# Optimization experiments

Hardware: AMD Instinct MI355X
Metric: run time of the kernel (lower is better)

## Reference

```python
import jax, jax.numpy as jnp
import numpy as np

NP, NT, H, FT, E, EL = 200000, 100000, 64, 64, 2000000, 500000


def _seg_mean(msg, dst, n):
    s = jax.ops.segment_sum(msg, dst, num_segments=n)
    c = jax.ops.segment_sum(jnp.ones(dst.shape, msg.dtype), dst, num_segments=n)
    return s / jnp.maximum(c, 1.0)[:, None]


def _sage(x_src, x_dst, src, dst, wl, bl, wr):
    # PyG SAGEConv (aggr='mean'): lin_l(mean_neighbors) + lin_r(x_dst); lin_r has no bias
    mean = _seg_mean(x_src[src], dst, x_dst.shape[0])
    return mean @ wl + bl + x_dst @ wr


def setup_inputs() -> dict:
    key = jax.random.key(0)
    ks = jax.random.split(key, 24)
    s = 1.0 / np.sqrt(H)
    inp = {
        "x_taxon": jax.random.normal(ks[0], (NT, FT), jnp.float32),
        "taxon_lin_w": jax.random.normal(ks[1], (FT, H), jnp.float32) * (1.0 / np.sqrt(FT)),
        "taxon_lin_b": jax.random.normal(ks[2], (H,), jnp.float32) * 0.01,
        "palmprint_emb": jax.random.normal(ks[3], (NP, H), jnp.float32),
        "taxon_emb": jax.random.normal(ks[4], (NT, H), jnp.float32),
        "n_id_palmprint": jnp.arange(NP, dtype=jnp.int64),
        "n_id_taxon": jnp.arange(NT, dtype=jnp.int64),
        "edge_src": jax.random.randint(ks[5], (E,), 0, NP, jnp.int64),
        "edge_dst": jax.random.randint(ks[6], (E,), 0, NT, jnp.int64),
        "el_src": jax.random.randint(ks[7], (EL,), 0, NP, jnp.int64),
        "el_dst": jax.random.randint(ks[8], (EL,), 0, NT, jnp.int64),
    }
    names = ["c1pt_wl", "c1pt_wr", "c1tp_wl", "c1tp_wr", "c2pt_wl", "c2pt_wr", "c2tp_wl", "c2tp_wr"]
    for i, nm in enumerate(names):
        inp[nm] = jax.random.normal(ks[9 + i], (H, H), jnp.float32) * s
    for i, nm in enumerate(["c1pt_bl", "c1tp_bl", "c2pt_bl", "c2tp_bl"]):
        inp[nm] = jax.random.normal(ks[17 + i], (H,), jnp.float32) * 0.01
    return inp


def reference(x_taxon, taxon_lin_w, taxon_lin_b, palmprint_emb, taxon_emb,
              c1pt_wl, c1pt_wr, c1tp_wl, c1tp_wr, c2pt_wl, c2pt_wr, c2tp_wl, c2tp_wr,
              c1pt_bl, c1tp_bl, c2pt_bl, c2tp_bl,
              n_id_palmprint, n_id_taxon, edge_src, edge_dst, el_src, el_dst):
    # initial features (use_embeddings=True)
    x_p = palmprint_emb[n_id_palmprint]                       # [NP, H]
    x_t = x_taxon @ taxon_lin_w + taxon_lin_b + taxon_emb[n_id_taxon]  # [NT, H]

    # layer 1: p->t and t->p (reverse edges), then ReLU
    t1 = _sage(x_p, x_t, edge_src, edge_dst, c1pt_wl, c1pt_bl, c1pt_wr)
    p1 = _sage(x_t, x_p, edge_dst, edge_src, c1tp_wl, c1tp_bl, c1tp_wr)
    p1, t1 = jax.nn.relu(p1), jax.nn.relu(t1)

    # layer 2
    t2 = _sage(p1, t1, edge_src, edge_dst, c2pt_wl, c2pt_bl, c2pt_wr)
    p2 = _sage(t1, p1, edge_dst, edge_src, c2tp_wl, c2tp_bl, c2tp_wr)

    # classifier: per-supervision-edge dot product
    return jnp.sum(p2[el_src] * t2[el_dst], axis=-1)          # [EL]
```

## Files before the change

### kernel.cpp

```cpp
#include <hip/hip_runtime.h>

#define H 64
#define EPB 4096
#define BMAX 400
#define ST 256
#define SP 512
#define LSHT 18
#define LSHP 17
#define CAPB 5632

typedef _Float16 half2v __attribute__((ext_vector_type(2)));
typedef _Float16 half8v __attribute__((ext_vector_type(8)));
typedef _Float16 f16x8  __attribute__((ext_vector_type(8)));
typedef float    f32x4  __attribute__((ext_vector_type(4)));
typedef int      i32x4  __attribute__((ext_vector_type(4)));

#if defined(__has_builtin)
#if __has_builtin(__builtin_amdgcn_fdot2)
#define HAS_FDOT2 1
#endif
#endif

#define MFMA16(a, b, c) __builtin_amdgcn_mfma_f32_16x16x32_f16(a, b, c, 0, 0, 0)

template <int HALF_IN>
__device__ __forceinline__ void mfma_dual_dev(const void* __restrict__ Av,
                                              const float* __restrict__ W1,
                                              const float* __restrict__ W2,
                                              const float* __restrict__ b2,
                                              _Float16* __restrict__ C1,
                                              _Float16* __restrict__ C2,
                                              int N, int wid, int nwaves) {
    const int lane = threadIdx.x & 63;
    const int m = lane & 15, quad = lane >> 4;
    const int nTiles = (N + 15) >> 4;

    f16x8 w1f[2][4], w2f[2][4];
#pragma unroll
    for (int kh = 0; kh < 2; ++kh)
#pragma unroll
        for (int nt = 0; nt < 4; ++nt) {
            f16x8 a, b;
#pragma unroll
            for (int j = 0; j < 8; ++j) {
                int k = kh * 32 + quad * 8 + j;
                a[j] = (_Float16)W1[k * 64 + nt * 16 + m];
                b[j] = (_Float16)W2[k * 64 + nt * 16 + m];
            }
            w1f[kh][nt] = a;
            w2f[kh][nt] = b;
        }
    float bv[4];
#pragma unroll
    for (int nt = 0; nt < 4; ++nt) bv[nt] = b2[nt * 16 + m];

    for (int t = wid; t < nTiles; t += nwaves) {
        int row = t * 16 + m;
        f16x8 alo = {}, ahi = {};
        if (row < N) {
            if (HALF_IN) {
                const f16x8* A8 = (const f16x8*)Av;
                alo = __builtin_nontemporal_load(A8 + (size_t)row * 8 + quad);
                ahi = __builtin_nontemporal_load(A8 + (size_t)row * 8 + 4 + quad);
            } else {
                const f32x4* p = (const f32x4*)((const float*)Av + (size_t)row * 64);
                f32x4 x0 = __builtin_nontemporal_load(p + quad * 2);
                f32x4 x1 = __builtin_nontemporal_load(p + quad * 2 + 1);
                f32x4 x2 = __builtin_nontemporal_load(p + 8 + quad * 2);
                f32x4 x3 = __builtin_nontemporal_load(p + 8 + quad * 2 + 1);
                alo[0] = (_Float16)x0[0]; alo[1] = (_Float16)x0[1];
                alo[2] = (_Float16)x0[2]; alo[3] = (_Float16)x0[3];
                alo[4] = (_Float16)x1[0]; alo[5] = (_Float16)x1[1];
                alo[6] = (_Float16)x1[2]; alo[7] = (_Float16)x1[3];
                ahi[0] = (_Float16)x2[0]; ahi[1] = (_Float16)x2[1];
                ahi[2] = (_Float16)x2[2]; ahi[3] = (_Float16)x2[3];
                ahi[4] = (_Float16)x3[0]; ahi[5] = (_Float16)x3[1];
                ahi[6] = (_Float16)x3[2]; ahi[7] = (_Float16)x3[3];
            }
        }
#pragma unroll
        for (int nt = 0; nt < 4; ++nt) {
            f32x4 a1 = {0.f, 0.f, 0.f, 0.f}, a2 = {0.f, 0.f, 0.f, 0.f};
            a1 = MFMA16(alo, w1f[0][nt], a1);
            a1 = MFMA16(ahi, w1f[1][nt], a1);
            a2 = MFMA16(alo, w2f[0][nt], a2);
            a2 = MFMA16(ahi, w2f[1][nt], a2);
#pragma unroll
            for (int r = 0; r < 4; ++r) {
                int orow = t * 16 + quad * 4 + r;
                if (orow < N) {
                    C1[(size_t)orow * 64 + nt * 16 + m] = (_Float16)a1[r];
                    C2[(size_t)orow * 64 + nt * 16 + m] = (_Float16)(a2[r] + bv[nt]);
                }
            }
        }
    }
}

__device__ __forceinline__ void mfma_xt_dev(const float* __restrict__ A,
                                            const float* __restrict__ W,
                                            const float* __restrict__ bias,
                                            const float* __restrict__ addend,
                                            _Float16* __restrict__ C,
                                            int N, int wid, int nwaves) {
    const int lane = threadIdx.x & 63;
    const int m = lane & 15, quad = lane >> 4;
    const int nTiles = (N + 15) >> 4;

    f16x8 wf[2][4];
#pragma unroll
    for (int kh = 0; kh < 2; ++kh)
#pragma unroll
        for (int nt = 0; nt < 4; ++nt) {
            f16x8 a;
#pragma unroll
            for (int j = 0; j < 8; ++j) {
                int k = kh * 32 + quad * 8 + j;
                a[j] = (_Float16)W[k * 64 + nt * 16 + m];
            }
            wf[kh][nt] = a;
        }
    float bv[4];
#pragma unroll
    for (int nt = 0; nt < 4; ++nt) bv[nt] = bias[nt * 16 + m];

    for (int t = wid; t < nTiles; t += nwaves) {
        int row = t * 16 + m;
        f16x8 alo = {}, ahi = {};
        if (row < N) {
            const f32x4* p = (const f32x4*)(A + (size_t)row * 64);
            f32x4 x0 = __builtin_nontemporal_load(p + quad * 2);
            f32x4 x1 = __builtin_nontemporal_load(p + quad * 2 + 1);
            f32x4 x2 = __builtin_nontemporal_load(p + 8 + quad * 2);
            f32x4 x3 = __builtin_nontemporal_load(p + 8 + quad * 2 + 1);
            alo[0] = (_Float16)x0[0]; alo[1] = (_Float16)x0[1];
            alo[2] = (_Float16)x0[2]; alo[3] = (_Float16)x0[3];
            alo[4] = (_Float16)x1[0]; alo[5] = (_Float16)x1[1];
            alo[6] = (_Float16)x1[2]; alo[7] = (_Float16)x1[3];
            ahi[0] = (_Float16)x2[0]; ahi[1] = (_Float16)x2[1];
            ahi[2] = (_Float16)x2[2]; ahi[3] = (_Float16)x2[3];
            ahi[4] = (_Float16)x3[0]; ahi[5] = (_Float16)x3[1];
            ahi[6] = (_Float16)x3[2]; ahi[7] = (_Float16)x3[3];
        }
#pragma unroll
        for (int nt = 0; nt < 4; ++nt) {
            f32x4 a1 = {0.f, 0.f, 0.f, 0.f};
            a1 = MFMA16(alo, wf[0][nt], a1);
            a1 = MFMA16(ahi, wf[1][nt], a1);
#pragma unroll
            for (int r = 0; r < 4; ++r) {
                int orow = t * 16 + quad * 4 + r;
                if (orow < N) {
                    float ad = __builtin_nontemporal_load(
                        &addend[(size_t)orow * 64 + nt * 16 + m]);
                    C[(size_t)orow * 64 + nt * 16 + m] = (_Float16)(a1[r] + bv[nt] + ad);
                }
            }
        }
    }
}

__device__ __forceinline__ void block_scan512(int* sc, int tid) {
    for (int off = 1; off < 512; off <<= 1) {
        int i0 = tid, i1 = tid + 256;
        int v0 = (i0 >= off) ? sc[i0 - off] : 0;
        int v1 = (i1 >= off) ? sc[i1 - off] : 0;
        __syncthreads();
        sc[i0] += v0;
        sc[i1] += v1;
        __syncthreads();
    }
}

__global__ void __launch_bounds__(256) k_bin_xt(
    const int* __restrict__ src, const int* __restrict__ dst,
    int* __restrict__ curT, int* __restrict__ curP,
    unsigned* __restrict__ binT, unsigned* __restrict__ binP,
    int BT, int BP, int E, int nbBin,
    const float* __restrict__ A, const float* __restrict__ W,
    const float* __restrict__ bias, const float* __restrict__ addend,
    _Float16* __restrict__ C, int NT_, int xtBlocks) {
    __shared__ int cT[BMAX], cP[BMAX], oT[BMAX], oP[BMAX], cur[BMAX];
    __shared__ int sc[512];
    __shared__ unsigned stage[EPB];
    int tid = threadIdx.x;
    if ((int)blockIdx.x >= nbBin) {
        int xb = blockIdx.x - nbBin;
        mfma_xt_dev(A, W, bias, addend, C, NT_, xb * 4 + (tid >> 6), xtBlocks * 4);
        return;
    }
    const int wave = tid >> 6, lane = tid & 63;
    for (int i = tid; i < BMAX; i += 256) { cT[i] = 0; cP[i] = 0; }
    __syncthreads();
    int e0 = blockIdx.x * EPB;
    int ls[EPB / 256], ld[EPB / 256];
#pragma unroll
    for (int k = 0; k < EPB / 256; ++k) {
        int i = e0 + k * 256 + tid;
        if (i < E) {
            ls[k] = __builtin_nontemporal_load(&src[i]);
            ld[k] = __builtin_nontemporal_load(&dst[i]);
            atomicAdd(&cT[ld[k] >> 8], 1);
            atomicAdd(&cP[ls[k] >> 9], 1);
        }
    }
    __syncthreads();
    for (int b = tid; b < BT; b += 256) { int c = cT[b]; oT[b] = c ? atomicAdd(&curT[b], c) : 0; }
    for (int b = tid; b < BP; b += 256) { int c = cP[b]; oP[b] = c ? atomicAdd(&curP[b], c) : 0; }
    sc[tid]       = (tid < BT) ? cT[tid] : 0;
    sc[tid + 256] = (tid + 256 < BT) ? cT[tid + 256] : 0;
    __syncthreads();
    block_scan512(sc, tid);
    for (int b = tid; b < BT; b += 256) cur[b] = sc[b] - cT[b];
    __syncthreads();
#pragma unroll
    for (int k = 0; k < EPB / 256; ++k) {
        int i = e0 + k * 256 + tid;
        if (i < E) {
            int bt = ld[k] >> 8;
            int pos = atomicAdd(&cur[bt], 1);
            stage[pos] = ((unsigned)(ld[k] & 255) << LSHT) | (unsigned)ls[k];
        }
    }
    __syncthreads();
    for (int b = wave; b < BT; b += 4) {
        int cnt = cT[b], so = sc[b] - cnt, go = oT[b];
        for (int i = lane; i < cnt; i += 64) {
            int pos = go + i;
            if (pos < CAPB) binT[(size_t)b * CAPB + pos] = stage[so + i];
        }
    }
    __syncthreads();
    sc[tid]       = (tid < BP) ? cP[tid] : 0;
    sc[tid + 256] = (tid + 256 < BP) ? cP[tid + 256] : 0;
    __syncthreads();
    block_scan512(sc, tid);
    for (int b = tid; b < BP; b += 256) cur[b] = sc[b] - cP[b];
    __syncthreads();
#pragma unroll
    for (int k = 0; k < EPB / 256; ++k) {
        int i = e0 + k * 256 + tid;
        if (i < E) {
            int bp = ls[k] >> 9;
            int pos = atomicAdd(&cur[bp], 1);
            stage[pos] = ((unsigned)(ls[k] & 511) << LSHP) | (unsigned)ld[k];
        }
    }
    __syncthreads();
    for (int b = wave; b < BP; b += 4) {
        int cnt = cP[b], so = sc[b] - cnt, go = oP[b];
        for (int i = lane; i < cnt; i += 64) {
            int pos = go + i;
            if (pos < CAPB) binP[(size_t)b * CAPB + pos] = stage[so + i];
        }
    }
}

__device__ __forceinline__ void csr_dev(const unsigned* __restrict__ binned,
                                        const int* __restrict__ cur,
                                        int* __restrict__ start_g, int* __restrict__ cnt_g,
                                        int* __restrict__ adj,
                                        int S, int lshift, int N, int b,
                                        int* lcnt, int* lscan, int* lcur, int* adj_lds) {
    int tid = threadIdx.x;
    int base = b * CAPB;
    int n = cur[b]; if (n > CAPB) n = CAPB;
    int rowlo = b * S;
    unsigned nbmask = (1u << lshift) - 1u;

    for (int i = tid; i < S; i += 256) lcnt[i] = 0;
    __syncthreads();
    for (int i = tid; i < n; i += 256)
        atomicAdd(&lcnt[binned[base + i] >> lshift], 1);
    __syncthreads();
    for (int i = tid; i < S; i += 256) lscan[i] = lcnt[i];
    __syncthreads();
    for (int off = 1; off < S; off <<= 1) {
        int i0 = tid, i1 = tid + 256;
        int v0 = (i0 >= off) ? lscan[i0 - off] : 0;
        int v1 = (S > 256 && i1 >= off) ? lscan[i1 - off] : 0;
        __syncthreads();
        if (i0 < S) lscan[i0] += v0;
        if (S > 256 && i1 < S) lscan[i1] += v1;
        __syncthreads();
    }
    for (int r = tid; r < S; r += 256) {
        int ex = lscan[r] - lcnt[r];
        lcur[r] = ex;
        int row = rowlo + r;
        if (row < N) {
            start_g[row] = base + ex;
            cnt_g[row]   = lcnt[r];
        }
    }
    __syncthreads();
    for (int i = tid; i < n; i += 256) {
        unsigned e = binned[base + i];
        int r = e >> lshift;
        int pos = atomicAdd(&lcur[r], 1);
        adj_lds[pos] = (int)(e & nbmask);
    }
    __syncthreads();
    int n4 = n & ~3;
    for (int i = tid * 4; i < n4; i += 1024)
        *(int4*)&adj[base + i] = *(const int4*)&adj_lds[i];
    for (int i = n4 + tid; i < n; i += 256)
        adj[base + i] = adj_lds[i];
}

__global__ void __launch_bounds__(256) k_csr_mfma1(
    const unsigned* __restrict__ binT, const unsigned* __restrict__ binP,
    const int* __restrict__ curT, const int* __restrict__ curP,
    int* __restrict__ start_t, int* __restrict__ cnt_t, int* __restrict__ adj_t,
    int* __restrict__ start_p, int* __restrict__ cnt_p, int* __restrict__ adj_p,
    int BT, int BP, int NT_, int NP_,
    const _Float16* __restrict__ XTh, const float* __restrict__ Wt1, const float* __restrict__ Wt2,
    const float* __restrict__ bt2, _Float16* __restrict__ Aht, _Float16* __restrict__ Bth,
    const float* __restrict__ pemb, const float* __restrict__ Wp1, const float* __restrict__ Wp2,
    const float* __restrict__ bp2, _Float16* __restrict__ Ahp, _Float16* __restrict__ Bph,
    int tB, int pB) {
    __shared__ int lcnt[512], lscan[512], lcur[512];
    __shared__ int adj_lds[CAPB];
    int bi = blockIdx.x;
    if (bi < BT) {
        csr_dev(binT, curT, start_t, cnt_t, adj_t, ST, LSHT, NT_, bi, lcnt, lscan, lcur, adj_lds);
    } else if (bi < BT + BP) {
        csr_dev(binP, curP, start_p, cnt_p, adj_p, SP, LSHP, NP_, bi - BT, lcnt, lscan, lcur, adj_lds);
    } else if (bi < BT + BP + tB) {
        int wb = bi - BT - BP;
        mfma_dual_dev<1>(XTh, Wt1, Wt2, bt2, Aht, Bth, NT_, wb * 4 + (threadIdx.x >> 6), tB * 4);
    } else {
        int wb = bi - BT - BP - tB;
        mfma_dual_dev<0>(pemb, Wp1, Wp2, bp2, Ahp, Bph, NP_, wb * 4 + (threadIdx.x >> 6), pB * 4);
    }
}

__device__ __forceinline__ void stage_w_lds(half8v* ldsW,
                                            const float* __restrict__ W1,
                                            const float* __restrict__ W2, int tid) {
    for (int f = tid; f < 1024; f += 256) {
        int lane = f & 63, nt = (f >> 6) & 3, kh = (f >> 8) & 1, tbl = f >> 9;
        int m = lane & 15, quad = lane >> 4;
        const float* W = tbl ? W2 : W1;
        half8v frag;
#pragma unroll
        for (int j = 0; j < 8; ++j) {
            int k = kh * 32 + quad * 8 + j;
            frag[j] = (_Float16)W[k * 64 + nt * 16 + m];
        }
        ldsW[f] = frag;
    }
}

__device__ __forceinline__ void gather_gemm_dev(
    const int* __restrict__ adj, const int* __restrict__ start, const int* __restrict__ cnt,
    const _Float16* __restrict__ A, const _Float16* __restrict__ B,
    const half8v* __restrict__ ldsW, const float* __restrict__ b2,
    _Float16* __restrict__ C1, _Float16* __restrict__ C2,
    int N, int tile) {
    const int lane = threadIdx.x & 63;
    const int m = lane & 15, quad = lane >> 4;
    const int row = tile * 16 + m;

    half8v accl = {}, acch = {};
    int dg = 0;
    if (row < N) {
        int st = start[row];
        dg     = cnt[row];
        const half8v* A8 = (const half8v*)A;
        int j = 0;
        for (; j + 7 < dg; j += 8) {
            int n[8];
#pragma unroll
            for (int k = 0; k < 8; ++k) n[k] = adj[st + j + k];
            half8v lv[8], hv[8];
#pragma unroll
            for (int k = 0; k < 8; ++k) {
                const half8v* rp = A8 + (size_t)n[k] * 8 + quad;
                lv[k] = rp[0];
                hv[k] = rp[4];
            }
            accl += ((lv[0] + lv[1]) + (lv[2] + lv[3])) + ((lv[4] + lv[5]) + (lv[6] + lv[7]));
            acch += ((hv[0] + hv[1]) + (hv[2] + hv[3])) + ((hv[4] + hv[5]) + (hv[6] + hv[7]));
        }
        if (j + 3 < dg) {
            int n[4];
#pragma unroll
            for (int k = 0; k < 4; ++k) n[k] = adj[st + j + k];
            half8v lv[4], hv[4];
#pragma unroll
            for (int k = 0; k < 4; ++k) {
                const half8v* rp = A8 + (size_t)n[k] * 8 + quad;
                lv[k] = rp[0];
                hv[k] = rp[4];
            }
            accl += (lv[0] + lv[1]) + (lv[2] + lv[3]);
            acch += (hv[0] + hv[1]) + (hv[2] + hv[3]);
            j += 4;
        }
        for (; j < dg; ++j) {
            const half8v* rp = A8 + (size_t)adj[st + j] * 8 + quad;
            accl += rp[0];
            acch += rp[4];
        }
    }

    f16x8 alo = {}, ahi = {};
    if (row < N) {
        float inv = 1.0f / (float)(dg > 1 ? dg : 1);
        half8v bl = __builtin_nontemporal_load(&((const half8v*)B)[(size_t)row * 8 + quad]);
        half8v bh = __builtin_nontemporal_load(&((const half8v*)B)[(size_t)row * 8 + 4 + quad]);
#pragma unroll
        for (int k = 0; k < 8; ++k) {
            float vl = fmaxf((float)accl[k] * inv + (float)bl[k], 0.f);
            float vh = fmaxf((float)acch[k] * inv + (float)bh[k], 0.f);
            alo[k] = (_Float16)vl;
            ahi[k] = (_Float16)vh;
        }
    }

#pragma unroll
    for (int nt = 0; nt < 4; ++nt) {
        f16x8 w1l = (f16x8)ldsW[(0 * 8 + 0 * 4 + nt) * 64 + lane];
        f16x8 w1h = (f16x8)ldsW[(0 * 8 + 1 * 4 + nt) * 64 + lane];
        f16x8 w2l = (f16x8)ldsW[(1 * 8 + 0 * 4 + nt) * 64 + lane];
        f16x8 w2h = (f16x8)ldsW[(1 * 8 + 1 * 4 + nt) * 64 + lane];
        f32x4 a1 = {0.f, 0.f, 0.f, 0.f}, a2 = {0.f, 0.f, 0.f, 0.f};
        a1 = MFMA16(alo, w1l, a1);
        a1 = MFMA16(ahi, w1h, a1);
        a2 = MFMA16(alo, w2l, a2);
        a2 = MFMA16(ahi, w2h, a2);
        float bb = b2[nt * 16 + m];
#pragma unroll
        for (int r = 0; r < 4; ++r) {
            int orow = tile * 16 + quad * 4 + r;
            if (orow < N) {
                C1[(size_t)orow * 64 + nt * 16 + m] = (_Float16)a1[r];
                C2[(size_t)orow * 64 + nt * 16 + m] = (_Float16)(a2[r] + bb);
            }
        }
    }
}

__global__ void __launch_bounds__(256) k_gather_gemm(
    const int* __restrict__ adjT, const int* __restrict__ startT, const int* __restrict__ cntT,
    const _Float16* __restrict__ At, const _Float16* __restrict__ Bt,
    const float* __restrict__ Wt1, const float* __restrict__ Wt2, const float* __restrict__ bt2,
    _Float16* __restrict__ C1t, _Float16* __restrict__ C2t, int NT_,
    const int* __restrict__ adjP, const int* __restrict__ startP, const int* __restrict__ cntP,
    const _Float16* __restrict__ Ap, const _Float16* __restrict__ Bp,
    const float* __restrict__ Wp1, const float* __restrict__ Wp2, const float* __restrict__ bp2,
    _Float16* __restrict__ C1p, _Float16* __restrict__ C2p, int NP_,
    int tTB) {
    __shared__ half8v ldsW[1024];
    const int tid = threadIdx.x, wave = tid >> 6;
    if ((int)blockIdx.x < tTB) {
        stage_w_lds(ldsW, Wt1, Wt2, tid);
        __syncthreads();
        int tile = blockIdx.x * 4 + wave;
        if (tile < ((NT_ + 15) >> 4))
            gather_gemm_dev(adjT, startT, cntT, At, Bt, ldsW, bt2, C1t, C2t, NT_, tile);
    } else {
        stage_w_lds(ldsW, Wp1, Wp2, tid);
        __syncthreads();
        int tile = (blockIdx.x - tTB) * 4 + wave;
        if (tile < ((NP_ + 15) >> 4))
            gather_gemm_dev(adjP, startP, cntP, Ap, Bp, ldsW, bp2, C1p, C2p, NP_, tile);
    }
}

__device__ __forceinline__ void gather_dev(
    const int* __restrict__ adj, const int* __restrict__ start, const int* __restrict__ cnt,
    const _Float16* __restrict__ A, const _Float16* __restrict__ B,
    _Float16* __restrict__ out, int do_relu, int N, int gidx) {
    int row = gidx >> 3;
    int c   = gidx & 7;
    if (row >= N) return;

    int st = start[row];
    int dg = cnt[row];
    const half8v* A8 = (const half8v*)A;
    half8v acc = {};
    int j = 0;
    for (; j + 15 < dg; j += 16) {
        int n[16];
#pragma unroll
        for (int k = 0; k < 16; ++k) n[k] = adj[st + j + k];
        half8v v[16];
#pragma unroll
        for (int k = 0; k < 16; ++k) v[k] = A8[(size_t)n[k] * 8 + c];
        half8v s0 = ((v[0] + v[1]) + (v[2] + v[3])) + ((v[4] + v[5]) + (v[6] + v[7]));
        half8v s1 = ((v[8] + v[9]) + (v[10] + v[11])) + ((v[12] + v[13]) + (v[14] + v[15]));
        acc += s0 + s1;
    }
    if (j + 7 < dg) {
        int n[8];
#pragma unroll
        for (int k = 0; k < 8; ++k) n[k] = adj[st + j + k];
        half8v v[8];
#pragma unroll
        for (int k = 0; k < 8; ++k) v[k] = A8[(size_t)n[k] * 8 + c];
        acc += ((v[0] + v[1]) + (v[2] + v[3])) + ((v[4] + v[5]) + (v[6] + v[7]));
        j += 8;
    }
    if (j + 3 < dg) {
        int n[4];
#pragma unroll
        for (int k = 0; k < 4; ++k) n[k] = adj[st + j + k];
        half8v v[4];
#pragma unroll
        for (int k = 0; k < 4; ++k) v[k] = A8[(size_t)n[k] * 8 + c];
        acc += (v[0] + v[1]) + (v[2] + v[3]);
        j += 4;
    }
    for (; j < dg; ++j)
        acc += A8[(size_t)adj[st + j] * 8 + c];

    float inv = 1.0f / (float)(dg > 1 ? dg : 1);
    half8v b8 = __builtin_nontemporal_load(&((const half8v*)B)[(size_t)row * 8 + c]);
    half8v o;
#pragma unroll
    for (int k = 0; k < 8; ++k) {
        float v = (float)acc[k] * inv + (float)b8[k];
        if (do_relu) v = fmaxf(v, 0.f);
        o[k] = (_Float16)v;
    }
    ((half8v*)out)[(size_t)row * 8 + c] = o;
}

__global__ void __launch_bounds__(256) k_gather2(
    const int* __restrict__ adjT, const int* __restrict__ startT, const int* __restrict__ cntT,
    const _Float16* __restrict__ At, const _Float16* __restrict__ Bt, _Float16* __restrict__ outT, int NT_,
    const int* __restrict__ adjP, const int* __restrict__ startP, const int* __restrict__ cntP,
    const _Float16* __restrict__ Ap, const _Float16* __restrict__ Bp, _Float16* __restrict__ outP, int NP_,
    int do_relu, int wTb) {
    if ((int)blockIdx.x < wTb)
        gather_dev(adjT, startT, cntT, At, Bt, outT, do_relu, NT_, blockIdx.x * 256 + threadIdx.x);
    else
        gather_dev(adjP, startP, cntP, Ap, Bp, outP, do_relu, NP_,
                   (blockIdx.x - wTb) * 256 + threadIdx.x);
}

__global__ void __launch_bounds__(256) dot_h(const _Float16* __restrict__ p2,
                                             const _Float16* __restrict__ t2,
                                             const int* __restrict__ els,
                                             const int* __restrict__ eld,
                                             float* __restrict__ out, int EL) {
    int tid = blockIdx.x * 256 + threadIdx.x;
    int i = tid >> 3, c = tid & 7;
    if (i < EL) {
        int s = __builtin_nontemporal_load(&els[i]);
        int d = __builtin_nontemporal_load(&eld[i]);
        half8v a = ((const half8v*)p2)[(size_t)s * 8 + c];
        half8v b = ((const half8v*)t2)[(size_t)d * 8 + c];
        float v = 0.f;
#ifdef HAS_FDOT2
        const half2v* ap = (const half2v*)&a;
        const half2v* bp = (const half2v*)&b;
#pragma unroll
        for (int k = 0; k < 4; ++k) v = __builtin_amdgcn_fdot2(ap[k], bp[k], v, false);
#else
#pragma unroll
        for (int k = 0; k < 8; ++k) v += (float)a[k] * (float)b[k];
#endif
        v += __shfl_xor(v, 1, 64);
        v += __shfl_xor(v, 2, 64);
        v += __shfl_xor(v, 4, 64);
        if (c == 0) __builtin_nontemporal_store(v, &out[i]);
    }
}

extern "C" void kernel_launch(void* const* d_in, const int* in_sizes, int n_in,
                              void* d_out, int out_size, void* d_ws, size_t ws_size,
                              hipStream_t stream) {
    const float* x_taxon  = (const float*)d_in[0];
    const float* tlw      = (const float*)d_in[1];
    const float* tlb      = (const float*)d_in[2];
    const float* pemb     = (const float*)d_in[3];
    const float* temb     = (const float*)d_in[4];
    const int*   edge_src = (const int*)d_in[7];
    const int*   edge_dst = (const int*)d_in[8];
    const int*   el_src   = (const int*)d_in[9];
    const int*   el_dst   = (const int*)d_in[10];
    const float* c1pt_wl  = (const float*)d_in[11];
    const float* c1pt_wr  = (const float*)d_in[12];
    const float* c1tp_wl  = (const float*)d_in[13];
    const float* c1tp_wr  = (const float*)d_in[14];
    const float* c2pt_wl  = (const float*)d_in[15];
    const float* c2pt_wr  = (const float*)d_in[16];
    const float* c2tp_wl  = (const float*)d_in[17];
    const float* c2tp_wr  = (const float*)d_in[18];
    const float* c1pt_bl  = (const float*)d_in[19];
    const float* c1tp_bl  = (const float*)d_in[20];
    const float* c2pt_bl  = (const float*)d_in[21];
    const float* c2tp_bl  = (const float*)d_in[22];

    const int NP_ = in_sizes[5];
    const int NT_ = in_sizes[6];
    const int E_  = in_sizes[7];
    const int EL_ = in_sizes[9];
    const int BT  = (NT_ + ST - 1) / ST;
    const int BP  = (NP_ + SP - 1) / SP;

    _Float16* hb   = (_Float16*)d_ws;
    _Float16* XTh  = hb;
    _Float16* Aht1 = XTh + (size_t)NT_ * H;
    _Float16* Bth1 = Aht1 + (size_t)NT_ * H;
    _Float16* Bth2 = Bth1 + (size_t)NT_ * H;
    _Float16* Ahp1 = Bth2 + (size_t)NT_ * H;
    _Float16* Bph1 = Ahp1 + (size_t)NP_ * H;
    _Float16* Ahp2 = Bph1 + (size_t)NP_ * H;
    _Float16* Bph2 = Ahp2 + (size_t)NP_ * H;
    _Float16* Aht2 = XTh;
    _Float16* T2h  = Aht1;
    _Float16* P2h  = Ahp1;

    unsigned* binT    = (unsigned*)(Bph2 + (size_t)NP_ * H);
    unsigned* binP    = binT + (size_t)BT * CAPB;
    int*      adj_t   = (int*)(binP + (size_t)BP * CAPB);
    int*      adj_p   = adj_t + (size_t)BT * CAPB;
    int* start_t = adj_p + (size_t)BP * CAPB;
    int* start_p = start_t + NT_;
    int* cnt_t   = start_p + NP_;
    int* cnt_p   = cnt_t + NT_;
    int* curT    = cnt_p + NP_;
    int* curP    = curT + BMAX;

    (void)hipMemsetAsync(curT, 0, 2 * BMAX * sizeof(int), stream);

    const int nbBin = (E_ + EPB - 1) / EPB;
    const int XTB   = 512;
    const int wT = (NT_ * 8 + 255) / 256, wP = (NP_ * 8 + 255) / 256;
    const int tB = 256, pB = 512;

    k_bin_xt<<<nbBin + XTB, 256, 0, stream>>>(
        edge_src, edge_dst, curT, curP, binT, binP, BT, BP, E_, nbBin,
        x_taxon, tlw, tlb, temb, XTh, NT_, XTB);

    k_csr_mfma1<<<BT + BP + tB + pB, 256, 0, stream>>>(
        binT, binP, curT, curP,
        start_t, cnt_t, adj_t, start_p, cnt_p, adj_p, BT, BP, NT_, NP_,
        XTh, c1tp_wl, c1pt_wr, c1pt_bl, Aht1, Bth1,
        pemb, c1pt_wl, c1tp_wr, c1tp_bl, Ahp1, Bph1, tB, pB);

    const int tTB = (((NT_ + 15) >> 4) + 3) >> 2;
    const int pTB = (((NP_ + 15) >> 4) + 3) >> 2;
    k_gather_gemm<<<tTB + pTB, 256, 0, stream>>>(
        adj_t, start_t, cnt_t, Ahp1, Bth1, c2tp_wl, c2pt_wr, c2pt_bl, Aht2, Bth2, NT_,
        adj_p, start_p, cnt_p, Aht1, Bph1, c2pt_wl, c2tp_wr, c2tp_bl, Ahp2, Bph2, NP_,
        tTB);

    k_gather2<<<wT + wP, 256, 0, stream>>>(
        adj_t, start_t, cnt_t, Ahp2, Bth2, T2h, NT_,
        adj_p, start_p, cnt_p, Aht2, Bph2, P2h, NP_, 0, wT);

    dot_h<<<(EL_ * 8 + 255) / 256, 256, 0, stream>>>(P2h, T2h, el_src, el_dst,
                                                     (float*)d_out, EL_);
}
```

Baseline: 476.7 us.

## Aggregate-then-transform both SAGE layers with fused gather-GEMM kernels

The old path projected features through both weight matrices first, then gathered projected rows, and ran a separate gather-only pass for layer 2. Now raw fp16 features are gathered and mean-aggregated, then one fused MFMA applies lin_l and lin_r together, with output staged through LDS for coalesced stores. Palmprint embeddings are cast to fp16 inside the binning kernel, the standalone projection work in the CSR kernel is dropped, and intermediate buffers shrink. This removes a full pass over edges and several intermediate tensors, but the layer-1 gather now waits on CSR completion with no projection overlap.

```diff
diff --git a/kernel.cpp b/kernel.cpp
--- a/kernel.cpp
+++ b/kernel.cpp
@@ -22,80 +22,6 @@
 #endif
 
 #define MFMA16(a, b, c) __builtin_amdgcn_mfma_f32_16x16x32_f16(a, b, c, 0, 0, 0)
-
-template <int HALF_IN>
-__device__ __forceinline__ void mfma_dual_dev(const void* __restrict__ Av,
-                                              const float* __restrict__ W1,
-                                              const float* __restrict__ W2,
-                                              const float* __restrict__ b2,
-                                              _Float16* __restrict__ C1,
-                                              _Float16* __restrict__ C2,
-                                              int N, int wid, int nwaves) {
-    const int lane = threadIdx.x & 63;
-    const int m = lane & 15, quad = lane >> 4;
-    const int nTiles = (N + 15) >> 4;
-
-    f16x8 w1f[2][4], w2f[2][4];
-#pragma unroll
-    for (int kh = 0; kh < 2; ++kh)
-#pragma unroll
-        for (int nt = 0; nt < 4; ++nt) {
-            f16x8 a, b;
-#pragma unroll
-            for (int j = 0; j < 8; ++j) {
-                int k = kh * 32 + quad * 8 + j;
-                a[j] = (_Float16)W1[k * 64 + nt * 16 + m];
-                b[j] = (_Float16)W2[k * 64 + nt * 16 + m];
-            }
-            w1f[kh][nt] = a;
-            w2f[kh][nt] = b;
-        }
-    float bv[4];
-#pragma unroll
-    for (int nt = 0; nt < 4; ++nt) bv[nt] = b2[nt * 16 + m];
-
-    for (int t = wid; t < nTiles; t += nwaves) {
-        int row = t * 16 + m;
-        f16x8 alo = {}, ahi = {};
-        if (row < N) {
-            if (HALF_IN) {
-                const f16x8* A8 = (const f16x8*)Av;
-                alo = __builtin_nontemporal_load(A8 + (size_t)row * 8 + quad);
-                ahi = __builtin_nontemporal_load(A8 + (size_t)row * 8 + 4 + quad);
-            } else {
-                const f32x4* p = (const f32x4*)((const float*)Av + (size_t)row * 64);
-                f32x4 x0 = __builtin_nontemporal_load(p + quad * 2);
-                f32x4 x1 = __builtin_nontemporal_load(p + quad * 2 + 1);
-                f32x4 x2 = __builtin_nontemporal_load(p + 8 + quad * 2);
-                f32x4 x3 = __builtin_nontemporal_load(p + 8 + quad * 2 + 1);
-                alo[0] = (_Float16)x0[0]; alo[1] = (_Float16)x0[1];
-                alo[2] = (_Float16)x0[2]; alo[3] = (_Float16)x0[3];
-                alo[4] = (_Float16)x1[0]; alo[5] = (_Float16)x1[1];
-                alo[6] = (_Float16)x1[2]; alo[7] = (_Float16)x1[3];
-                ahi[0] = (_Float16)x2[0]; ahi[1] = (_Float16)x2[1];
-                ahi[2] = (_Float16)x2[2]; ahi[3] = (_Float16)x2[3];
-                ahi[4] = (_Float16)x3[0]; ahi[5] = (_Float16)x3[1];
-                ahi[6] = (_Float16)x3[2]; ahi[7] = (_Float16)x3[3];
-            }
-        }
-#pragma unroll
-        for (int nt = 0; nt < 4; ++nt) {
-            f32x4 a1 = {0.f, 0.f, 0.f, 0.f}, a2 = {0.f, 0.f, 0.f, 0.f};
-            a1 = MFMA16(alo, w1f[0][nt], a1);
-            a1 = MFMA16(ahi, w1f[1][nt], a1);
-            a2 = MFMA16(alo, w2f[0][nt], a2);
-            a2 = MFMA16(ahi, w2f[1][nt], a2);
-#pragma unroll
-            for (int r = 0; r < 4; ++r) {
-                int orow = t * 16 + quad * 4 + r;
-                if (orow < N) {
-                    C1[(size_t)orow * 64 + nt * 16 + m] = (_Float16)a1[r];
-                    C2[(size_t)orow * 64 + nt * 16 + m] = (_Float16)(a2[r] + bv[nt]);
-                }
-            }
-        }
-    }
-}
 
 __device__ __forceinline__ void mfma_xt_dev(const float* __restrict__ A,
                                             const float* __restrict__ W,
@@ -179,11 +105,30 @@
     int BT, int BP, int E, int nbBin,
     const float* __restrict__ A, const float* __restrict__ W,
     const float* __restrict__ bias, const float* __restrict__ addend,
-    _Float16* __restrict__ C, int NT_, int xtBlocks) {
+    _Float16* __restrict__ C, int NT_, int xtBlocks,
+    const float* __restrict__ pembIn, _Float16* __restrict__ PhOut,
+    int NP_, int castBlocks) {
     __shared__ int cT[BMAX], cP[BMAX], oT[BMAX], oP[BMAX], cur[BMAX];
     __shared__ int sc[512];
     __shared__ unsigned stage[EPB];
     int tid = threadIdx.x;
+    if ((int)blockIdx.x >= nbBin + xtBlocks) {
+        int cb = blockIdx.x - nbBin - xtBlocks;
+        int idx = cb * 256 + tid, stride = castBlocks * 256;
+        int total = NP_ * 8;
+        for (int i = idx; i < total; i += stride) {
+            const f32x4* p = (const f32x4*)(pembIn + (size_t)i * 8);
+            f32x4 x0 = __builtin_nontemporal_load(p);
+            f32x4 x1 = __builtin_nontemporal_load(p + 1);
+            f16x8 o;
+            o[0] = (_Float16)x0[0]; o[1] = (_Float16)x0[1];
+            o[2] = (_Float16)x0[2]; o[3] = (_Float16)x0[3];
+            o[4] = (_Float16)x1[0]; o[5] = (_Float16)x1[1];
+            o[6] = (_Float16)x1[2]; o[7] = (_Float16)x1[3];
+            *(f16x8*)&PhOut[(size_t)i * 8] = o;
+        }
+        return;
+    }
     if ((int)blockIdx.x >= nbBin) {
         int xb = blockIdx.x - nbBin;
         mfma_xt_dev(A, W, bias, addend, C, NT_, xb * 4 + (tid >> 6), xtBlocks * 4);
@@ -308,31 +253,19 @@
         adj[base + i] = adj_lds[i];
 }
 
-__global__ void __launch_bounds__(256) k_csr_mfma1(
+__global__ void __launch_bounds__(256) k_csr(
     const unsigned* __restrict__ binT, const unsigned* __restrict__ binP,
     const int* __restrict__ curT, const int* __restrict__ curP,
     int* __restrict__ start_t, int* __restrict__ cnt_t, int* __restrict__ adj_t,
     int* __restrict__ start_p, int* __restrict__ cnt_p, int* __restrict__ adj_p,
-    int BT, int BP, int NT_, int NP_,
-    const _Float16* __restrict__ XTh, const float* __restrict__ Wt1, const float* __restrict__ Wt2,
-    const float* __restrict__ bt2, _Float16* __restrict__ Aht, _Float16* __restrict__ Bth,
-    const float* __restrict__ pemb, const float* __restrict__ Wp1, const float* __restrict__ Wp2,
-    const float* __restrict__ bp2, _Float16* __restrict__ Ahp, _Float16* __restrict__ Bph,
-    int tB, int pB) {
+    int BT, int BP, int NT_, int NP_) {
     __shared__ int lcnt[512], lscan[512], lcur[512];
     __shared__ int adj_lds[CAPB];
     int bi = blockIdx.x;
-    if (bi < BT) {
+    if (bi < BT)
         csr_dev(binT, curT, start_t, cnt_t, adj_t, ST, LSHT, NT_, bi, lcnt, lscan, lcur, adj_lds);
-    } else if (bi < BT + BP) {
+    else
         csr_dev(binP, curP, start_p, cnt_p, adj_p, SP, LSHP, NP_, bi - BT, lcnt, lscan, lcur, adj_lds);
-    } else if (bi < BT + BP + tB) {
-        int wb = bi - BT - BP;
-        mfma_dual_dev<1>(XTh, Wt1, Wt2, bt2, Aht, Bth, NT_, wb * 4 + (threadIdx.x >> 6), tB * 4);
-    } else {
-        int wb = bi - BT - BP - tB;
-        mfma_dual_dev<0>(pemb, Wp1, Wp2, bp2, Ahp, Bph, NP_, wb * 4 + (threadIdx.x >> 6), pB * 4);
-    }
 }
 
 __device__ __forceinline__ void stage_w_lds(half8v* ldsW,
@@ -352,12 +285,14 @@
     }
 }
 
-__device__ __forceinline__ void gather_gemm_dev(
+#define LDSC_STRIDE 72
+#define LDSC_TBL    1152
+__device__ __forceinline__ void gg_dev(
     const int* __restrict__ adj, const int* __restrict__ start, const int* __restrict__ cnt,
-    const _Float16* __restrict__ A, const _Float16* __restrict__ B,
-    const half8v* __restrict__ ldsW, const float* __restrict__ b2,
-    _Float16* __restrict__ C1, _Float16* __restrict__ C2,
-    int N, int tile) {
+    const _Float16* __restrict__ G, const _Float16* __restrict__ S,
+    const half8v* __restrict__ ldsW, _Float16* __restrict__ ldsC_w,
+    const float* __restrict__ bias,
+    _Float16* __restrict__ out, int N, int tile, int do_relu) {
     const int lane = threadIdx.x & 63;
     const int m = lane & 15, quad = lane >> 4;
     const int row = tile * 16 + m;
@@ -367,7 +302,7 @@
     if (row < N) {
         int st = start[row];
         dg     = cnt[row];
-        const half8v* A8 = (const half8v*)A;
+        const half8v* G8 = (const half8v*)G;
         int j = 0;
         for (; j + 7 < dg; j += 8) {
             int n[8];
@@ -376,7 +311,7 @@
             half8v lv[8], hv[8];
 #pragma unroll
             for (int k = 0; k < 8; ++k) {
-                const half8v* rp = A8 + (size_t)n[k] * 8 + quad;
+                const half8v* rp = G8 + (size_t)n[k] * 8 + quad;
                 lv[k] = rp[0];
                 hv[k] = rp[4];
             }
@@ -390,7 +325,7 @@
             half8v lv[4], hv[4];
 #pragma unroll
             for (int k = 0; k < 4; ++k) {
-                const half8v* rp = A8 + (size_t)n[k] * 8 + quad;
+                const half8v* rp = G8 + (size_t)n[k] * 8 + quad;
                 lv[k] = rp[0];
                 hv[k] = rp[4];
             }
@@ -399,146 +334,85 @@
             j += 4;
         }
         for (; j < dg; ++j) {
-            const half8v* rp = A8 + (size_t)adj[st + j] * 8 + quad;
+            const half8v* rp = G8 + (size_t)adj[st + j] * 8 + quad;
             accl += rp[0];
             acch += rp[4];
         }
     }
 
-    f16x8 alo = {}, ahi = {};
+    f16x8 alo = {}, ahi = {}, slo = {}, shi = {};
     if (row < N) {
         float inv = 1.0f / (float)(dg > 1 ? dg : 1);
-        half8v bl = __builtin_nontemporal_load(&((const half8v*)B)[(size_t)row * 8 + quad]);
-        half8v bh = __builtin_nontemporal_load(&((const half8v*)B)[(size_t)row * 8 + 4 + quad]);
 #pragma unroll
         for (int k = 0; k < 8; ++k) {
-            float vl = fmaxf((float)accl[k] * inv + (float)bl[k], 0.f);
-            float vh = fmaxf((float)acch[k] * inv + (float)bh[k], 0.f);
-            alo[k] = (_Float16)vl;
-            ahi[k] = (_Float16)vh;
-        }
+            alo[k] = (_Float16)((float)accl[k] * inv);
+            ahi[k] = (_Float16)((float)acch[k] * inv);
+        }
+        const f16x8* S8 = (const f16x8*)S;
+        slo = S8[(size_t)row * 8 + quad];
+        shi = S8[(size_t)row * 8 + 4 + quad];
     }
 
 #pragma unroll
     for (int nt = 0; nt < 4; ++nt) {
-        f16x8 w1l = (f16x8)ldsW[(0 * 8 + 0 * 4 + nt) * 64 + lane];
-        f16x8 w1h = (f16x8)ldsW[(0 * 8 + 1 * 4 + nt) * 64 + lane];
-        f16x8 w2l = (f16x8)ldsW[(1 * 8 + 0 * 4 + nt) * 64 + lane];
-        f16x8 w2h = (f16x8)ldsW[(1 * 8 + 1 * 4 + nt) * 64 + lane];
-        f32x4 a1 = {0.f, 0.f, 0.f, 0.f}, a2 = {0.f, 0.f, 0.f, 0.f};
-        a1 = MFMA16(alo, w1l, a1);
-        a1 = MFMA16(ahi, w1h, a1);
-        a2 = MFMA16(alo, w2l, a2);
-        a2 = MFMA16(ahi, w2h, a2);
-        float bb = b2[nt * 16 + m];
+        f16x8 wl_lo = (f16x8)ldsW[(0 * 8 + 0 * 4 + nt) * 64 + lane];
+        f16x8 wl_hi = (f16x8)ldsW[(0 * 8 + 1 * 4 + nt) * 64 + lane];
+        f16x8 wr_lo = (f16x8)ldsW[(1 * 8 + 0 * 4 + nt) * 64 + lane];
+        f16x8 wr_hi = (f16x8)ldsW[(1 * 8 + 1 * 4 + nt) * 64 + lane];
+        f32x4 a = {0.f, 0.f, 0.f, 0.f};
+        a = MFMA16(alo, wl_lo, a);
+        a = MFMA16(ahi, wl_hi, a);
+        a = MFMA16(slo, wr_lo, a);
+        a = MFMA16(shi, wr_hi, a);
+        float bb = bias[nt * 16 + m];
 #pragma unroll
         for (int r = 0; r < 4; ++r) {
-            int orow = tile * 16 + quad * 4 + r;
-            if (orow < N) {
-                C1[(size_t)orow * 64 + nt * 16 + m] = (_Float16)a1[r];
-                C2[(size_t)orow * 64 + nt * 16 + m] = (_Float16)(a2[r] + bb);
+            float v = a[r] + bb;
+            if (do_relu) v = fmaxf(v, 0.f);
+            ldsC_w[(quad * 4 + r) * LDSC_STRIDE + nt * 16 + m] = (_Float16)v;
+        }
+    }
+
+    {
+        int rl = lane >> 2, ch = lane & 3;
+        int orow = tile * 16 + rl;
+        if (orow < N) {
+#pragma unroll
+            for (int half = 0; half < 2; ++half) {
+                int lo = rl * LDSC_STRIDE + ch * 8 + half * 32;
+                f16x8 v = *(const f16x8*)&ldsC_w[lo];
+                *(f16x8*)&out[(size_t)orow * 64 + ch * 8 + half * 32] = v;
             }
         }
     }
 }
 
-__global__ void __launch_bounds__(256) k_gather_gemm(
+__global__ void __launch_bounds__(256) k_gg(
     const int* __restrict__ adjT, const int* __restrict__ startT, const int* __restrict__ cntT,
-    const _Float16* __restrict__ At, const _Float16* __restrict__ Bt,
-    const float* __restrict__ Wt1, const float* __restrict__ Wt2, const float* __restrict__ bt2,
-    _Float16* __restrict__ C1t, _Float16* __restrict__ C2t, int NT_,
+    const _Float16* __restrict__ Gt, const _Float16* __restrict__ St,
+    const float* __restrict__ Wlt, const float* __restrict__ Wrt, const float* __restrict__ bt,
+    _Float16* __restrict__ outT, int NT_,
     const int* __restrict__ adjP, const int* __restrict__ startP, const int* __restrict__ cntP,
-    const _Float16* __restrict__ Ap, const _Float16* __restrict__ Bp,
-    const float* __restrict__ Wp1, const float* __restrict__ Wp2, const float* __restrict__ bp2,
-    _Float16* __restrict__ C1p, _Float16* __restrict__ C2p, int NP_,
-    int tTB) {
+    const _Float16* __restrict__ Gp, const _Float16* __restrict__ Sp,
+    const float* __restrict__ Wlp, const float* __restrict__ Wrp, const float* __restrict__ bp,
+    _Float16* __restrict__ outP, int NP_,
+    int tTB, int do_relu) {
     __shared__ half8v ldsW[1024];
+    __shared__ __align__(16) _Float16 ldsC[4][LDSC_TBL];
     const int tid = threadIdx.x, wave = tid >> 6;
     if ((int)blockIdx.x < tTB) {
-        stage_w_lds(ldsW, Wt1, Wt2, tid);
+        stage_w_lds(ldsW, Wlt, Wrt, tid);
         __syncthreads();
         int tile = blockIdx.x * 4 + wave;
         if (tile < ((NT_ + 15) >> 4))
-            gather_gemm_dev(adjT, startT, cntT, At, Bt, ldsW, bt2, C1t, C2t, NT_, tile);
+            gg_dev(adjT, startT, cntT, Gt, St, ldsW, ldsC[wave], bt, outT, NT_, tile, do_relu);
     } else {
-        stage_w_lds(ldsW, Wp1, Wp2, tid);
+        stage_w_lds(ldsW, Wlp, Wrp, tid);
         __syncthreads();
         int tile = (blockIdx.x - tTB) * 4 + wave;
         if (tile < ((NP_ + 15) >> 4))
-            gather_gemm_dev(adjP, startP, cntP, Ap, Bp, ldsW, bp2, C1p, C2p, NP_, tile);
-    }
-}
-
-__device__ __forceinline__ void gather_dev(
-    const int* __restrict__ adj, const int* __restrict__ start, const int* __restrict__ cnt,
-    const _Float16* __restrict__ A, const _Float16* __restrict__ B,
-    _Float16* __restrict__ out, int do_relu, int N, int gidx) {
-    int row = gidx >> 3;
-    int c   = gidx & 7;
-    if (row >= N) return;
-
-    int st = start[row];
-    int dg = cnt[row];
-    const half8v* A8 = (const half8v*)A;
-    half8v acc = {};
-    int j = 0;
-    for (; j + 15 < dg; j += 16) {
-        int n[16];
-#pragma unroll
-        for (int k = 0; k < 16; ++k) n[k] = adj[st + j + k];
-        half8v v[16];
-#pragma unroll
-        for (int k = 0; k < 16; ++k) v[k] = A8[(size_t)n[k] * 8 + c];
-        half8v s0 = ((v[0] + v[1]) + (v[2] + v[3])) + ((v[4] + v[5]) + (v[6] + v[7]));
-        half8v s1 = ((v[8] + v[9]) + (v[10] + v[11])) + ((v[12] + v[13]) + (v[14] + v[15]));
-        acc += s0 + s1;
-    }
-    if (j + 7 < dg) {
-        int n[8];
-#pragma unroll
-        for (int k = 0; k < 8; ++k) n[k] = adj[st + j + k];
-        half8v v[8];
-#pragma unroll
-        for (int k = 0; k < 8; ++k) v[k] = A8[(size_t)n[k] * 8 + c];
-        acc += ((v[0] + v[1]) + (v[2] + v[3])) + ((v[4] + v[5]) + (v[6] + v[7]));
-        j += 8;
-    }
-    if (j + 3 < dg) {
-        int n[4];
-#pragma unroll
-        for (int k = 0; k < 4; ++k) n[k] = adj[st + j + k];
-        half8v v[4];
-#pragma unroll
-        for (int k = 0; k < 4; ++k) v[k] = A8[(size_t)n[k] * 8 + c];
-        acc += (v[0] + v[1]) + (v[2] + v[3]);
-        j += 4;
-    }
-    for (; j < dg; ++j)
-        acc += A8[(size_t)adj[st + j] * 8 + c];
-
-    float inv = 1.0f / (float)(dg > 1 ? dg : 1);
-    half8v b8 = __builtin_nontemporal_load(&((const half8v*)B)[(size_t)row * 8 + c]);
-    half8v o;
-#pragma unroll
-    for (int k = 0; k < 8; ++k) {
-        float v = (float)acc[k] * inv + (float)b8[k];
-        if (do_relu) v = fmaxf(v, 0.f);
-        o[k] = (_Float16)v;
-    }
-    ((half8v*)out)[(size_t)row * 8 + c] = o;
-}
-
-__global__ void __launch_bounds__(256) k_gather2(
-    const int* __restrict__ adjT, const int* __restrict__ startT, const int* __restrict__ cntT,
-    const _Float16* __restrict__ At, const _Float16* __restrict__ Bt, _Float16* __restrict__ outT, int NT_,
-    const int* __restrict__ adjP, const int* __restrict__ startP, const int* __restrict__ cntP,
-    const _Float16* __restrict__ Ap, const _Float16* __restrict__ Bp, _Float16* __restrict__ outP, int NP_,
-    int do_relu, int wTb) {
-    if ((int)blockIdx.x < wTb)
-        gather_dev(adjT, startT, cntT, At, Bt, outT, do_relu, NT_, blockIdx.x * 256 + threadIdx.x);
-    else
-        gather_dev(adjP, startP, cntP, Ap, Bp, outP, do_relu, NP_,
-                   (blockIdx.x - wTb) * 256 + threadIdx.x);
+            gg_dev(adjP, startP, cntP, Gp, Sp, ldsW, ldsC[wave], bp, outP, NP_, tile, do_relu);
+    }
 }
 
 __global__ void __launch_bounds__(256) dot_h(const _Float16* __restrict__ p2,
@@ -602,20 +476,15 @@
     const int BT  = (NT_ + ST - 1) / ST;
     const int BP  = (NP_ + SP - 1) / SP;
 
-    _Float16* hb   = (_Float16*)d_ws;
-    _Float16* XTh  = hb;
-    _Float16* Aht1 = XTh + (size_t)NT_ * H;
-    _Float16* Bth1 = Aht1 + (size_t)NT_ * H;
-    _Float16* Bth2 = Bth1 + (size_t)NT_ * H;
-    _Float16* Ahp1 = Bth2 + (size_t)NT_ * H;
-    _Float16* Bph1 = Ahp1 + (size_t)NP_ * H;
-    _Float16* Ahp2 = Bph1 + (size_t)NP_ * H;
-    _Float16* Bph2 = Ahp2 + (size_t)NP_ * H;
-    _Float16* Aht2 = XTh;
-    _Float16* T2h  = Aht1;
-    _Float16* P2h  = Ahp1;
-
-    unsigned* binT    = (unsigned*)(Bph2 + (size_t)NP_ * H);
+    _Float16* hb  = (_Float16*)d_ws;
+    _Float16* XTh = hb;
+    _Float16* Ph  = XTh + (size_t)NT_ * H;
+    _Float16* t1  = Ph + (size_t)NP_ * H;
+    _Float16* p1  = t1 + (size_t)NT_ * H;
+    _Float16* t2  = XTh;
+    _Float16* p2  = Ph;
+
+    unsigned* binT    = (unsigned*)(p1 + (size_t)NP_ * H);
     unsigned* binP    = binT + (size_t)BT * CAPB;
     int*      adj_t   = (int*)(binP + (size_t)BP * CAPB);
     int*      adj_p   = adj_t + (size_t)BT * CAPB;
@@ -630,30 +499,29 @@
 
     const int nbBin = (E_ + EPB - 1) / EPB;
     const int XTB   = 512;
-    const int wT = (NT_ * 8 + 255) / 256, wP = (NP_ * 8 + 255) / 256;
-    const int tB = 256, pB = 512;
-
-    k_bin_xt<<<nbBin + XTB, 256, 0, stream>>>(
+    const int CASTB = 256;
+
+    k_bin_xt<<<nbBin + XTB + CASTB, 256, 0, stream>>>(
         edge_src, edge_dst, curT, curP, binT, binP, BT, BP, E_, nbBin,
-        x_taxon, tlw, tlb, temb, XTh, NT_, XTB);
-
-    k_csr_mfma1<<<BT + BP + tB + pB, 256, 0, stream>>>(
+        x_taxon, tlw, tlb, temb, XTh, NT_, XTB, pemb, Ph, NP_, CASTB);
+
+    k_csr<<<BT + BP, 256, 0, stream>>>(
         binT, binP, curT, curP,
-        start_t, cnt_t, adj_t, start_p, cnt_p, adj_p, BT, BP, NT_, NP_,
-        XTh, c1tp_wl, c1pt_wr, c1pt_bl, Aht1, Bth1,
-        pemb, c1pt_wl, c1tp_wr, c1tp_bl, Ahp1, Bph1, tB, pB);
+        start_t, cnt_t, adj_t, start_p, cnt_p, adj_p, BT, BP, NT_, NP_);
 
     const int tTB = (((NT_ + 15) >> 4) + 3) >> 2;
     const int pTB = (((NP_ + 15) >> 4) + 3) >> 2;
-    k_gather_gemm<<<tTB + pTB, 256, 0, stream>>>(
-        adj_t, start_t, cnt_t, Ahp1, Bth1, c2tp_wl, c2pt_wr, c2pt_bl, Aht2, Bth2, NT_,
-        adj_p, start_p, cnt_p, Aht1, Bph1, c2pt_wl, c2tp_wr, c2tp_bl, Ahp2, Bph2, NP_,
-        tTB);
-
-    k_gather2<<<wT + wP, 256, 0, stream>>>(
-        adj_t, start_t, cnt_t, Ahp2, Bth2, T2h, NT_,
-        adj_p, start_p, cnt_p, Aht2, Bph2, P2h, NP_, 0, wT);
-
-    dot_h<<<(EL_ * 8 + 255) / 256, 256, 0, stream>>>(P2h, T2h, el_src, el_dst,
+
+    k_gg<<<tTB + pTB, 256, 0, stream>>>(
+        adj_t, start_t, cnt_t, Ph, XTh, c1pt_wl, c1pt_wr, c1pt_bl, t1, NT_,
+        adj_p, start_p, cnt_p, XTh, Ph, c1tp_wl, c1tp_wr, c1tp_bl, p1, NP_,
+        tTB, 1);
+
+    k_gg<<<tTB + pTB, 256, 0, stream>>>(
+        adj_t, start_t, cnt_t, p1, t1, c2pt_wl, c2pt_wr, c2pt_bl, t2, NT_,
+        adj_p, start_p, cnt_p, t1, p1, c2tp_wl, c2tp_wr, c2tp_bl, p2, NP_,
+        tTB, 0);
+
+    dot_h<<<(EL_ * 8 + 255) / 256, 256, 0, stream>>>(p2, t2, el_src, el_dst,
                                                      (float*)d_out, EL_);
 }
```

New measurement: 446.7 us. 6.3% less time.
